# Kernel tuning notes

Hardware: AMD Instinct MI355X
Metric: run time of the kernel (lower is better)

## Reference

```python
import jax, jax.numpy as jnp
import numpy as np

B = 64
HIST_LEN, PRED_HORIZON = 10, 10
H = W = 200
RES = 0.1
INIT_X_IDX, INIT_Y_IDX = 100.0, 160.0
FRONT_EDGE, BACK_EDGE = 3.89, 1.043
HALF_BOX = (FRONT_EDGE + BACK_EDGE) / 2.0
CENTER_SHIFT = HALF_BOX - BACK_EDGE          # mid-circle shift along box heading
FRONT_SHIFT = 2.0 * HALF_BOX - 2.0 * BACK_EDGE
EMBED, HIDDEN, CNN_OUT, CNN_CH = 64, 128, 1000, 32
SIGMA = 1.8
THETA = 0.0


def setup_inputs() -> dict:
    key = jax.random.key(0)
    ks = jax.random.split(key, 16)
    def rn(k, shape, scale=0.02):
        return jax.random.normal(k, shape, dtype=jnp.float32) * scale
    return {
        "img_feature": jax.random.normal(ks[0], (B, 12, H, W), dtype=jnp.float32),
        "hist_points": rn(ks[1], (B, HIST_LEN, 4), 1.0),
        "hist_points_step": rn(ks[2], (B, HIST_LEN, 4), 0.1),
        "ego_rendering_heading": jax.random.uniform(ks[3], (B, 1), dtype=jnp.float32, maxval=2.0 * np.pi),
        "comp_w": rn(ks[4], (3, 12, 3, 3)),
        "comp_b": jnp.zeros((3,), jnp.float32),
        "cnn_w": rn(ks[5], (CNN_CH, 3, 3, 3)),
        "cnn_b": jnp.zeros((CNN_CH,), jnp.float32),
        "cnn_fc_w": rn(ks[6], (CNN_OUT, CNN_CH)),
        "cnn_fc_b": jnp.zeros((CNN_OUT,), jnp.float32),
        "embed_w": rn(ks[7], (EMBED, 4)),
        "embed_b": jnp.zeros((EMBED,), jnp.float32),
        "h0": rn(ks[8], (1, HIDDEN)),
        "c0": rn(ks[9], (1, HIDDEN)),
        "w_ih": rn(ks[10], (4 * HIDDEN, EMBED)),
        "w_hh": rn(ks[11], (4 * HIDDEN, HIDDEN)),
        "b_ih": jnp.zeros((4 * HIDDEN,), jnp.float32),
        "b_hh": jnp.zeros((4 * HIDDEN,), jnp.float32),
        "out_w": rn(ks[12], (4, HIDDEN + CNN_OUT)),
        "out_b": jnp.zeros((4,), jnp.float32),
    }


def _conv(x, w, b, stride):
    y = jax.lax.conv_general_dilated(x, w, (stride, stride), 'SAME',
                                     dimension_numbers=('NCHW', 'OIHW', 'NCHW'))
    return y + b[None, :, None, None]


def _forward(img_feature, hist_points, hist_points_step, ego_rendering_heading,
             comp_w, comp_b, cnn_w, cnn_b, cnn_fc_w, cnn_fc_b,
             embed_w, embed_b, h0, c0, w_ih, w_hh, b_ih, b_hh, out_w, out_b):
    bsz = img_feature.shape[0]
    # CNN encoder: 12->3 compression conv, then backbone (stand-in for mobilenet_v2) -> 1000-dim
    z = _conv(img_feature, comp_w, comp_b, 1)
    z = jax.nn.relu(_conv(z, cnn_w, cnn_b, 2))
    z = z.mean(axis=(2, 3))                       # (B, CNN_CH) global avg pool
    img_emb = z @ cnn_fc_w.T + cnn_fc_b           # (B, 1000)

    def lstm_cell(e, h, c):                       # pytorch gate order i, f, g, o
        g = e @ w_ih.T + b_ih + h @ w_hh.T + b_hh
        i, f, gg, o = jnp.split(g, 4, axis=-1)
        c2 = jax.nn.sigmoid(f) * c + jax.nn.sigmoid(i) * jnp.tanh(gg)
        return jax.nn.sigmoid(o) * jnp.tanh(c2), c2

    def embed(step):
        return jax.nn.relu(step @ embed_w.T + embed_b)

    h = jnp.tile(h0, (bsz, 1))
    c = jnp.tile(c0, (bsz, 1))

    # warm up LSTM on history displacements (torch loop t = 1 .. HIST_LEN-1)
    def hist_step(carry, step_t):
        h, c = carry
        h, c = lstm_cell(embed(step_t), h, c)
        return (h, c), None
    (h, c), _ = jax.lax.scan(hist_step, (h, c),
                             jnp.swapaxes(hist_points_step[:, 1:HIST_LEN], 0, 1))

    def pred_step(carry, _):
        h, c, pose = carry
        step = jnp.concatenate([h, img_emb], axis=1) @ out_w.T + out_b
        pose = pose + step
        h, c = lstm_cell(embed(step), h, c)
        return (h, c, pose), pose
    _, poses = jax.lax.scan(pred_step, (h, c, hist_points[:, HIST_LEN - 1]),
                            None, length=PRED_HORIZON)
    pred_traj = jnp.swapaxes(poses, 0, 1)         # (B, T, 4) == torch pred_traj[:, 1:, :]

    # three-circle gaussian rasterization, vectorized over all timesteps
    ego = ego_rendering_heading.reshape(bsz)      # (B,)
    x, y, hd = pred_traj[..., 0], pred_traj[..., 1], pred_traj[..., 2]
    box_heading = -hd - ego[:, None]              # (B, T)
    ho = -(ego - np.pi / 2.0)                     # heading_offset, (B,)
    cos_ho, sin_ho = jnp.cos(ho)[:, None], jnp.sin(ho)[:, None]
    px = INIT_X_IDX + (x * cos_ho - y * sin_ho) / RES   # rear center in image idx
    py = INIT_Y_IDX - (x * sin_ho + y * cos_ho) / RES
    cos_bh, sin_bh = jnp.cos(box_heading), jnp.sin(box_heading)

    # idx_mesh built with meshgrid indexing='ij' over (W, H); image is square
    gx, gy = jnp.meshgrid(jnp.arange(W, dtype=jnp.float32),
                          jnp.arange(H, dtype=jnp.float32), indexing='ij')
    ct, st = np.cos(THETA), np.sin(THETA)
    ga = ct * ct / (2 * SIGMA ** 2) + st * st / (2 * SIGMA ** 2)
    gb = -np.sin(2 * THETA) / (4 * SIGMA ** 2) + np.sin(2 * THETA) / (4 * SIGMA ** 2)
    gc = st * st / (2 * SIGMA ** 2) + ct * ct / (2 * SIGMA ** 2)

    def gauss(shift):
        cx = px + shift / RES * cos_bh            # (B, T)
        cy = py - shift / RES * sin_bh
        dx = gx[None, None] - cx[..., None, None] # (B, T, H, W)
        dy = gy[None, None] - cy[..., None, None]
        return jnp.exp(-(ga * dx * dx + 2 * gb * dx * dy + gc * dy * dy))

    boxes = jnp.maximum(gauss(0.0), jnp.maximum(gauss(CENTER_SHIFT), gauss(FRONT_SHIFT)))
    pred_boxs = boxes[:, :, None]                 # (B, T, 1, H, W)
    return pred_traj, pred_boxs


def reference(img_feature, hist_points, hist_points_step, ego_rendering_heading,
              comp_w, comp_b, cnn_w, cnn_b, cnn_fc_w, cnn_fc_b,
              embed_w, embed_b, h0, c0, w_ih, w_hh, b_ih, b_hh, out_w, out_b):
    return _forward(img_feature, hist_points, hist_points_step, ego_rendering_heading,
                    comp_w, comp_b, cnn_w, cnn_b, cnn_fc_w, cnn_fc_b,
                    embed_w, embed_b, h0, c0, w_ih, w_hh, b_ih, b_hh, out_w, out_b)
```

## Files before the change

### kernel.cpp

```cpp
#include <hip/hip_runtime.h>
#include <math.h>

#define NPAR 10

typedef _Float16 f16;
typedef f16 f16x2 __attribute__((ext_vector_type(2)));

__device__ __forceinline__ float dot2acc(f16x2 a, f16x2 b, float c){
#if __has_builtin(__builtin_amdgcn_fdot2)
  return __builtin_amdgcn_fdot2(a, b, c, false);
#else
  return c + (float)a[0]*(float)b[0] + (float)a[1]*(float)b[1];
#endif
}

__global__ __launch_bounds__(256) void k_conv1(const float* __restrict__ img,
    const float* __restrict__ cw, const float* __restrict__ cb,
    float* __restrict__ o){
  int b = blockIdx.y;
  int tile = blockIdx.x;
  int x = threadIdx.x;
  if (x >= 200) return;
  int y0 = tile*8;
  const float* ib = img + (size_t)b*480000;
  float* ob = o + (size_t)b*120000;
  float acc[3][8];
  #pragma unroll
  for (int oc=0;oc<3;++oc){
    float bz = cb[oc];
    #pragma unroll
    for (int r=0;r<8;++r) acc[oc][r] = bz;
  }
  bool xl = (x>0), xr = (x<199);
  for (int ci=0; ci<12; ++ci){
    const float* cbase = ib + ci*40000;
    float vL[10], vM[10], vR[10];
    #pragma unroll
    for (int rr=0; rr<10; ++rr){
      int iy = y0-1+rr;
      bool rok = (unsigned)iy < 200u;
      const float* rp = cbase + iy*200 + x;
      vL[rr] = (rok && xl) ? rp[-1] : 0.f;
      vM[rr] =  rok        ? rp[ 0] : 0.f;
      vR[rr] = (rok && xr) ? rp[ 1] : 0.f;
    }
    #pragma unroll
    for (int oc=0;oc<3;++oc){
      const float* wp = cw + oc*108 + ci*9;
      float w00=wp[0], w01=wp[1], w02=wp[2],
            w10=wp[3], w11=wp[4], w12=wp[5],
            w20=wp[6], w21=wp[7], w22=wp[8];
      #pragma unroll
      for (int r=0;r<8;++r){
        float s = acc[oc][r];
        s = fmaf(vL[r],   w00, s); s = fmaf(vM[r],   w01, s); s = fmaf(vR[r],   w02, s);
        s = fmaf(vL[r+1], w10, s); s = fmaf(vM[r+1], w11, s); s = fmaf(vR[r+1], w12, s);
        s = fmaf(vL[r+2], w20, s); s = fmaf(vM[r+2], w21, s); s = fmaf(vR[r+2], w22, s);
        acc[oc][r] = s;
      }
    }
  }
  #pragma unroll
  for (int oc=0;oc<3;++oc)
    #pragma unroll
    for (int r=0;r<8;++r)
      ob[oc*40000 + (y0+r)*200 + x] = acc[oc][r];
}

__global__ __launch_bounds__(512) void k_conv2(const float* __restrict__ c1,
    const float* __restrict__ w, const float* __restrict__ bias,
    float* __restrict__ part){
  int blk = blockIdx.x; int b = blk/NPAR, p = blk%NPAR;
  int t = threadIdx.x; int lane = t & 63, wv = t >> 6;
  const float* cbs = c1 + (size_t)b*3*40000;
  float acc[32];
  #pragma unroll
  for (int co=0;co<32;++co) acc[co]=0.f;
  for (int i=0;i<2;++i){
    int px = t + 512*i; if (px>=1000) break;
    int oy = p*10 + px/100; int ox = px % 100;
    float v[27];
    #pragma unroll
    for (int ci=0;ci<3;++ci){
      #pragma unroll
      for (int ky=0;ky<3;++ky){
        int iy = 2*oy+ky; bool rok = iy < 200;
        #pragma unroll
        for (int kx=0;kx<3;++kx){
          int ix = 2*ox+kx;
          v[ci*9+ky*3+kx] = (rok && ix<200) ? cbs[ci*40000 + iy*200 + ix] : 0.f;
        }
      }
    }
    #pragma unroll
    for (int co=0;co<32;++co){
      float s = bias[co];
      #pragma unroll
      for (int q=0;q<27;++q) s = fmaf(v[q], w[co*27+q], s);
      acc[co] += fmaxf(s, 0.f);
    }
  }
  __shared__ float wred[8][32];
  #pragma unroll
  for (int co=0;co<32;++co){
    float s = acc[co];
    #pragma unroll
    for (int off=32; off; off>>=1) s += __shfl_down(s, off, 64);
    if (lane==0) wred[wv][co] = s;
  }
  __syncthreads();
  if (t < 32){
    float s = 0.f;
    #pragma unroll
    for (int q=0;q<8;++q) s += wred[q][t];
    part[(b*NPAR+p)*32 + t] = s;
  }
}

__global__ __launch_bounds__(256) void k_fc(const float* __restrict__ part,
    const float* __restrict__ fcw, const float* __restrict__ fcb,
    const float* __restrict__ ow, const float* __restrict__ ob,
    float* __restrict__ const4){
  int b = blockIdx.x, t = threadIdx.x, lane = t&63, wv = t>>6;
  __shared__ float z[32];
  __shared__ float wred[4][4];
  if (t < 32){
    float s = 0.f;
    #pragma unroll
    for (int p=0;p<NPAR;++p) s += part[(b*NPAR+p)*32 + t];
    z[t] = s * (1.f/10000.f);
  }
  __syncthreads();
  float cp0=0.f, cp1=0.f, cp2=0.f, cp3=0.f;
  for (int o = t; o < 1000; o += 256){
    float s = fcb[o];
    #pragma unroll
    for (int k=0;k<32;++k) s = fmaf(fcw[o*32+k], z[k], s);
    cp0 = fmaf(s, ow[0*1128+128+o], cp0);
    cp1 = fmaf(s, ow[1*1128+128+o], cp1);
    cp2 = fmaf(s, ow[2*1128+128+o], cp2);
    cp3 = fmaf(s, ow[3*1128+128+o], cp3);
  }
  #pragma unroll
  for (int off=32; off; off>>=1){
    cp0 += __shfl_down(cp0, off, 64);
    cp1 += __shfl_down(cp1, off, 64);
    cp2 += __shfl_down(cp2, off, 64);
    cp3 += __shfl_down(cp3, off, 64);
  }
  if (lane==0){ wred[wv][0]=cp0; wred[wv][1]=cp1; wred[wv][2]=cp2; wred[wv][3]=cp3; }
  __syncthreads();
  if (t < 4){
    float s = ob[t];
    #pragma unroll
    for (int q=0;q<4;++q) s += wred[q][t];
    const4[b*4+t] = s;
  }
}

__global__ __launch_bounds__(256) void k_lstm(
    const float* __restrict__ hist_pts, const float* __restrict__ hist_step,
    const float* __restrict__ emb_w, const float* __restrict__ emb_b,
    const float* __restrict__ h0, const float* __restrict__ c0,
    const float* __restrict__ w_ih, const float* __restrict__ w_hh,
    const float* __restrict__ b_ih, const float* __restrict__ b_hh,
    const float* __restrict__ out_w, const float* __restrict__ out_b,
    const float* __restrict__ const4, float* __restrict__ traj){
  int b = blockIdx.x; int t = threadIdx.x; int lane = t&63, wv = t>>6;
  int u  = (t<128) ? t       : t-128;
  int j1 = (t<128) ? t       : 128+u;
  int j2 = (t<128) ? 256+t   : 384+u;

  f16x2 w1[96], w2[96];
  {
    const float2* r1 = (const float2*)(w_ih + j1*64);
    const float2* r2 = (const float2*)(w_ih + j2*64);
    #pragma unroll
    for (int p=0;p<32;++p){
      float2 a = r1[p], c = r2[p];
      w1[p] = f16x2{(f16)a.x, (f16)a.y};
      w2[p] = f16x2{(f16)c.x, (f16)c.y};
    }
    const float2* q1 = (const float2*)(w_hh + j1*128);
    const float2* q2 = (const float2*)(w_hh + j2*128);
    #pragma unroll
    for (int p=0;p<64;++p){
      float2 a = q1[p], c = q2[p];
      w1[32+p] = f16x2{(f16)a.x, (f16)a.y};
      w2[32+p] = f16x2{(f16)c.x, (f16)c.y};
    }
  }
  float bias1 = b_ih[j1] + b_hh[j1];
  float bias2 = b_ih[j2] + b_hh[j2];

  __shared__ f16x2 xl[96];
  __shared__ float e_lds[64], h_lds[128], a_lds[128];
  __shared__ float step_lds[4], wred4[4];

  float c_reg = (t>=128) ? c0[u] : 0.f;
  if (t < 128) h_lds[t] = h0[t];

  auto cell = [&](){
    __syncthreads();
    if (t < 32)      xl[t]    = f16x2{(f16)e_lds[2*t],        (f16)e_lds[2*t+1]};
    else if (t < 96){ int p=t-32; xl[t] = f16x2{(f16)h_lds[2*p], (f16)h_lds[2*p+1]}; }
    __syncthreads();
    float acc1 = bias1, acc2 = bias2;
    #pragma unroll
    for (int cc=0; cc<12; ++cc){
      f16x2 xv[8];
      #pragma unroll
      for (int q=0;q<8;++q) xv[q] = xl[cc*8+q];
      #pragma unroll
      for (int q=0;q<8;++q){
        acc1 = dot2acc(w1[cc*8+q], xv[q], acc1);
        acc2 = dot2acc(w2[cc*8+q], xv[q], acc2);
      }
    }
    if (t < 128){
      float ig = 1.f/(1.f+expf(-acc1));
      float gg = tanhf(acc2);
      a_lds[t] = ig*gg;
    }
    __syncthreads();
    if (t >= 128){
      float ff = 1.f/(1.f+expf(-acc1));
      float oo = 1.f/(1.f+expf(-acc2));
      c_reg = ff*c_reg + a_lds[u];
      h_lds[u] = oo * tanhf(c_reg);
    }
  };

  for (int s=1; s<10; ++s){
    if (t < 64){
      const float* hp = hist_step + (size_t)(b*10+s)*4;
      float e = emb_b[t]
              + emb_w[t*4+0]*hp[0] + emb_w[t*4+1]*hp[1]
              + emb_w[t*4+2]*hp[2] + emb_w[t*4+3]*hp[3];
      e_lds[t] = fmaxf(e, 0.f);
    }
    cell();
  }

  float pose = (t<4) ? hist_pts[(size_t)(b*10+9)*4 + t] : 0.f;
  float cst  = (t<4) ? const4[b*4+t] : 0.f;
  for (int it=0; it<10; ++it){
    __syncthreads();
    {
      const float* owr = out_w + wv*1128;
      float p_ = owr[2*lane]*h_lds[2*lane] + owr[2*lane+1]*h_lds[2*lane+1];
      #pragma unroll
      for (int off=32; off; off>>=1) p_ += __shfl_down(p_, off, 64);
      if (lane==0) wred4[wv] = p_;
    }
    __syncthreads();
    if (t < 4){
      float st = wred4[t] + cst;
      pose += st;
      traj[(size_t)(b*10+it)*4 + t] = pose;
      step_lds[t] = st;
    }
    __syncthreads();
    if (it < 9){
      if (t < 64){
        float e = emb_b[t]
                + emb_w[t*4+0]*step_lds[0] + emb_w[t*4+1]*step_lds[1]
                + emb_w[t*4+2]*step_lds[2] + emb_w[t*4+3]*step_lds[3];
        e_lds[t] = fmaxf(e, 0.f);
      }
      cell();
    }
  }
}

__global__ __launch_bounds__(256) void k_raster(const float* __restrict__ traj,
    const float* __restrict__ ego, float* __restrict__ boxes){
  int img = blockIdx.y;
  int b = img / 10;
  __shared__ float ctr[6];
  if (threadIdx.x == 0){
    float x  = traj[img*4+0];
    float y  = traj[img*4+1];
    float hd = traj[img*4+2];
    float eg = ego[b];
    float ho = 1.5707963267948966f - eg;
    float sho, cho; __sincosf(ho, &sho, &cho);
    float pxc = 100.f + (x*cho - y*sho)*10.f;
    float pyc = 160.f - (x*sho + y*cho)*10.f;
    float bh  = -hd - eg;
    float sbh, cbh; __sincosf(bh, &sbh, &cbh);
    const float CSH = 14.235f;
    const float FSH = 28.47f;
    ctr[0] = pxc;             ctr[1] = pyc;
    ctr[2] = pxc + CSH*cbh;   ctr[3] = pyc - CSH*sbh;
    ctr[4] = pxc + FSH*cbh;   ctr[5] = pyc - FSH*sbh;
  }
  __syncthreads();
  int f4 = blockIdx.x*256 + threadIdx.x;
  if (f4 >= 10000) return;
  int p0 = f4*4;
  int i = p0 / 200;
  int j = p0 % 200;
  float fi = (float)i, fj = (float)j;
  float c0x=ctr[0], c0y=ctr[1], c1x=ctr[2], c1y=ctr[3], c2x=ctr[4], c2y=ctr[5];
  float dx0 = fi-c0x, dx1 = fi-c1x, dx2 = fi-c2x;
  float A0 = dx0*dx0, A1 = dx1*dx1, A2 = dx2*dx2;
  const float GA = 0.15432098765432098f;
  float r[4];
  #pragma unroll
  for (int l=0;l<4;++l){
    float dj = fj + (float)l;
    float dy0 = dj-c0y, dy1 = dj-c1y, dy2 = dj-c2y;
    float d0 = fmaf(dy0,dy0,A0);
    float d1 = fmaf(dy1,dy1,A1);
    float d2 = fmaf(dy2,dy2,A2);
    float m = fminf(d0, fminf(d1,d2));
    r[l] = __expf(-m*GA);
  }
  *(float4*)(boxes + (size_t)img*40000 + p0) = make_float4(r[0],r[1],r[2],r[3]);
}

extern "C" void kernel_launch(void* const* d_in, const int* in_sizes, int n_in,
                              void* d_out, int out_size, void* d_ws, size_t ws_size,
                              hipStream_t stream) {
  (void)in_sizes; (void)n_in; (void)d_ws; (void)ws_size; (void)out_size;
  const float* img = (const float*)d_in[0];
  const float* hp  = (const float*)d_in[1];
  const float* hps = (const float*)d_in[2];
  const float* ego = (const float*)d_in[3];
  const float* cw  = (const float*)d_in[4];
  const float* cb  = (const float*)d_in[5];
  const float* c2w = (const float*)d_in[6];
  const float* c2b = (const float*)d_in[7];
  const float* fcw = (const float*)d_in[8];
  const float* fcb = (const float*)d_in[9];
  const float* ew  = (const float*)d_in[10];
  const float* eb  = (const float*)d_in[11];
  const float* h0  = (const float*)d_in[12];
  const float* c0  = (const float*)d_in[13];
  const float* wih = (const float*)d_in[14];
  const float* whh = (const float*)d_in[15];
  const float* bih = (const float*)d_in[16];
  const float* bhh = (const float*)d_in[17];
  const float* ow  = (const float*)d_in[18];
  const float* ob  = (const float*)d_in[19];

  float* out  = (float*)d_out;
  float* traj = out;
  float* S    = out + 2560;
  float* c1   = S;
  float* part = S + 7680000;
  float* cst4 = S + 7700480;

  hipLaunchKernelGGL(k_conv1, dim3(25, 64),  dim3(256), 0, stream, img, cw, cb, c1);
  hipLaunchKernelGGL(k_conv2, dim3(64*NPAR), dim3(512), 0, stream, c1, c2w, c2b, part);
  hipLaunchKernelGGL(k_fc,    dim3(64),      dim3(256), 0, stream, part, fcw, fcb, ow, ob, cst4);
  hipLaunchKernelGGL(k_lstm,  dim3(64),      dim3(256), 0, stream,
                     hp, hps, ew, eb, h0, c0, wih, whh, bih, bhh, ow, ob, cst4, traj);
  hipLaunchKernelGGL(k_raster, dim3(40, 640), dim3(256), 0, stream, traj, ego, S);
}
```

Before: 150.0 us.

## Fuse compression conv and strided backbone conv via shared-memory tile

Merges the 12->3 conv and the stride-2 32-channel conv into one kernel. Each block computes an 11-row band of the first conv output into shared memory, including a halo row, and the second conv plus ReLU and the partial pooling read from that band. This drops the global write and re-read of the 30 MB intermediate and one kernel launch. In exchange, every band recomputes one overlapping row of the first conv, and each block now runs two phases with fewer threads busy in the second.

```diff
diff --git a/kernel.cpp b/kernel.cpp
--- a/kernel.cpp
+++ b/kernel.cpp
@@ -1,7 +1,5 @@
 #include <hip/hip_runtime.h>
 #include <math.h>
-
-#define NPAR 10
 
 typedef _Float16 f16;
 typedef f16 f16x2 __attribute__((ext_vector_type(2)));
@@ -14,106 +12,107 @@
 #endif
 }
 
-__global__ __launch_bounds__(256) void k_conv1(const float* __restrict__ img,
-    const float* __restrict__ cw, const float* __restrict__ cb,
-    float* __restrict__ o){
-  int b = blockIdx.y;
-  int tile = blockIdx.x;
-  int x = threadIdx.x;
-  if (x >= 200) return;
-  int y0 = tile*8;
-  const float* ib = img + (size_t)b*480000;
-  float* ob = o + (size_t)b*120000;
-  float acc[3][8];
+__global__ __launch_bounds__(256) void k_convfused(
+    const float* __restrict__ img, const float* __restrict__ cw, const float* __restrict__ cb,
+    const float* __restrict__ w2, const float* __restrict__ b2,
+    float* __restrict__ part){
+  int b = blockIdx.y, ty = blockIdx.x;
+  int oy0 = ty*5;
+  int y1  = 2*oy0;
+  int t = threadIdx.x;
+  __shared__ float c1[3][11][204];
+
+  if (t < 200){
+    int x = t;
+    const float* ib = img + (size_t)b*480000;
+    float acc[3][11];
+    #pragma unroll
+    for (int oc=0;oc<3;++oc){
+      float bz = cb[oc];
+      #pragma unroll
+      for (int r=0;r<11;++r) acc[oc][r] = bz;
+    }
+    bool xl = (x>0), xr = (x<199);
+    for (int ci=0; ci<12; ++ci){
+      const float* cbase = ib + ci*40000 + x;
+      float vL[13], vM[13], vR[13];
+      #pragma unroll
+      for (int rr=0; rr<13; ++rr){
+        int iy = y1-1+rr;
+        bool rok = (unsigned)iy < 200u;
+        const float* rp = cbase + iy*200;
+        vL[rr] = (rok && xl) ? rp[-1] : 0.f;
+        vM[rr] =  rok        ? rp[ 0] : 0.f;
+        vR[rr] = (rok && xr) ? rp[ 1] : 0.f;
+      }
+      #pragma unroll
+      for (int oc=0;oc<3;++oc){
+        const float* wp = cw + oc*108 + ci*9;
+        float w00=wp[0], w01=wp[1], w02=wp[2],
+              w10=wp[3], w11=wp[4], w12=wp[5],
+              w20=wp[6], w21=wp[7], w22=wp[8];
+        #pragma unroll
+        for (int r=0;r<11;++r){
+          float s = acc[oc][r];
+          s = fmaf(vL[r],   w00, s); s = fmaf(vM[r],   w01, s); s = fmaf(vR[r],   w02, s);
+          s = fmaf(vL[r+1], w10, s); s = fmaf(vM[r+1], w11, s); s = fmaf(vR[r+1], w12, s);
+          s = fmaf(vL[r+2], w20, s); s = fmaf(vM[r+2], w21, s); s = fmaf(vR[r+2], w22, s);
+          acc[oc][r] = s;
+        }
+      }
+    }
+    #pragma unroll
+    for (int oc=0;oc<3;++oc)
+      #pragma unroll
+      for (int r=0;r<11;++r)
+        c1[oc][r][x] = acc[oc][r];
+  }
+  __syncthreads();
+
+  float a2[32];
   #pragma unroll
-  for (int oc=0;oc<3;++oc){
-    float bz = cb[oc];
-    #pragma unroll
-    for (int r=0;r<8;++r) acc[oc][r] = bz;
-  }
-  bool xl = (x>0), xr = (x<199);
-  for (int ci=0; ci<12; ++ci){
-    const float* cbase = ib + ci*40000;
-    float vL[10], vM[10], vR[10];
-    #pragma unroll
-    for (int rr=0; rr<10; ++rr){
-      int iy = y0-1+rr;
-      bool rok = (unsigned)iy < 200u;
-      const float* rp = cbase + iy*200 + x;
-      vL[rr] = (rok && xl) ? rp[-1] : 0.f;
-      vM[rr] =  rok        ? rp[ 0] : 0.f;
-      vR[rr] = (rok && xr) ? rp[ 1] : 0.f;
-    }
-    #pragma unroll
-    for (int oc=0;oc<3;++oc){
-      const float* wp = cw + oc*108 + ci*9;
-      float w00=wp[0], w01=wp[1], w02=wp[2],
-            w10=wp[3], w11=wp[4], w12=wp[5],
-            w20=wp[6], w21=wp[7], w22=wp[8];
-      #pragma unroll
-      for (int r=0;r<8;++r){
-        float s = acc[oc][r];
-        s = fmaf(vL[r],   w00, s); s = fmaf(vM[r],   w01, s); s = fmaf(vR[r],   w02, s);
-        s = fmaf(vL[r+1], w10, s); s = fmaf(vM[r+1], w11, s); s = fmaf(vR[r+1], w12, s);
-        s = fmaf(vL[r+2], w20, s); s = fmaf(vM[r+2], w21, s); s = fmaf(vR[r+2], w22, s);
-        acc[oc][r] = s;
-      }
-    }
-  }
-  #pragma unroll
-  for (int oc=0;oc<3;++oc)
-    #pragma unroll
-    for (int r=0;r<8;++r)
-      ob[oc*40000 + (y0+r)*200 + x] = acc[oc][r];
-}
-
-__global__ __launch_bounds__(512) void k_conv2(const float* __restrict__ c1,
-    const float* __restrict__ w, const float* __restrict__ bias,
-    float* __restrict__ part){
-  int blk = blockIdx.x; int b = blk/NPAR, p = blk%NPAR;
-  int t = threadIdx.x; int lane = t & 63, wv = t >> 6;
-  const float* cbs = c1 + (size_t)b*3*40000;
-  float acc[32];
-  #pragma unroll
-  for (int co=0;co<32;++co) acc[co]=0.f;
-  for (int i=0;i<2;++i){
-    int px = t + 512*i; if (px>=1000) break;
-    int oy = p*10 + px/100; int ox = px % 100;
-    float v[27];
-    #pragma unroll
-    for (int ci=0;ci<3;++ci){
-      #pragma unroll
-      for (int ky=0;ky<3;++ky){
-        int iy = 2*oy+ky; bool rok = iy < 200;
+  for (int co=0;co<32;++co) a2[co]=0.f;
+  if (t < 250){
+    #pragma unroll
+    for (int e=0;e<2;++e){
+      int px = t + 250*e;
+      int q = px/100, ox = px - q*100;
+      float v[27];
+      #pragma unroll
+      for (int ci=0;ci<3;++ci){
         #pragma unroll
-        for (int kx=0;kx<3;++kx){
-          int ix = 2*ox+kx;
-          v[ci*9+ky*3+kx] = (rok && ix<200) ? cbs[ci*40000 + iy*200 + ix] : 0.f;
+        for (int ky=0;ky<3;++ky){
+          int lr = 2*q+ky;
+          bool rok = (y1 + lr) < 200;
+          #pragma unroll
+          for (int kx=0;kx<3;++kx){
+            int ix = 2*ox+kx;
+            v[ci*9+ky*3+kx] = (rok && ix<200) ? c1[ci][lr][ix] : 0.f;
+          }
         }
       }
-    }
-    #pragma unroll
-    for (int co=0;co<32;++co){
-      float s = bias[co];
-      #pragma unroll
-      for (int q=0;q<27;++q) s = fmaf(v[q], w[co*27+q], s);
-      acc[co] += fmaxf(s, 0.f);
-    }
-  }
-  __shared__ float wred[8][32];
+      #pragma unroll
+      for (int co=0;co<32;++co){
+        float s = b2[co];
+        #pragma unroll
+        for (int qq=0;qq<27;++qq) s = fmaf(v[qq], w2[co*27+qq], s);
+        a2[co] += fmaxf(s, 0.f);
+      }
+    }
+  }
+  int lane = t&63, wv = t>>6;
+  __shared__ float wred[4][32];
   #pragma unroll
   for (int co=0;co<32;++co){
-    float s = acc[co];
+    float s = a2[co];
     #pragma unroll
     for (int off=32; off; off>>=1) s += __shfl_down(s, off, 64);
     if (lane==0) wred[wv][co] = s;
   }
   __syncthreads();
   if (t < 32){
-    float s = 0.f;
-    #pragma unroll
-    for (int q=0;q<8;++q) s += wred[q][t];
-    part[(b*NPAR+p)*32 + t] = s;
+    float s = wred[0][t]+wred[1][t]+wred[2][t]+wred[3][t];
+    part[(b*20+ty)*32 + t] = s;
   }
 }
 
@@ -127,7 +126,7 @@
   if (t < 32){
     float s = 0.f;
     #pragma unroll
-    for (int p=0;p<NPAR;++p) s += part[(b*NPAR+p)*32 + t];
+    for (int p=0;p<20;++p) s += part[(b*20+p)*32 + t];
     z[t] = s * (1.f/10000.f);
   }
   __syncthreads();
@@ -348,12 +347,11 @@
   float* out  = (float*)d_out;
   float* traj = out;
   float* S    = out + 2560;
-  float* c1   = S;
-  float* part = S + 7680000;
-  float* cst4 = S + 7700480;
-
-  hipLaunchKernelGGL(k_conv1, dim3(25, 64),  dim3(256), 0, stream, img, cw, cb, c1);
-  hipLaunchKernelGGL(k_conv2, dim3(64*NPAR), dim3(512), 0, stream, c1, c2w, c2b, part);
+  float* part = S;
+  float* cst4 = S + 40960;
+
+  hipLaunchKernelGGL(k_convfused, dim3(20, 64), dim3(256), 0, stream,
+                     img, cw, cb, c2w, c2b, part);
   hipLaunchKernelGGL(k_fc,    dim3(64),      dim3(256), 0, stream, part, fcw, fcb, ow, ob, cst4);
   hipLaunchKernelGGL(k_lstm,  dim3(64),      dim3(256), 0, stream,
                      hp, hps, ew, eb, h0, c0, wih, whh, bih, bhh, ow, ob, cst4, traj);
```

Result: slower. 155.3 us (+3.5%).
